# Kernel optimization log

Hardware: AMD Instinct MI355X
Metric: run time of the kernel (lower is better)

## Reference

```python
import jax, jax.numpy as jnp
import numpy as np
from jax.ops import segment_sum

N_NODES = 100000
N_EDGES = 1600000
IN_DIM, HID_DIM, OUT_DIM = 256, 128, 237


def setup_inputs() -> dict:
    key = jax.random.key(0)
    ks = jax.random.split(key, 6)
    x = jax.random.normal(ks[0], (N_NODES, IN_DIM), dtype=jnp.float32)
    edge_index = jax.random.randint(ks[1], (2, N_EDGES), 0, N_NODES, dtype=jnp.int64)
    # Glorot-style init like PyG GCNConv
    W1 = jax.random.normal(ks[2], (IN_DIM, HID_DIM), dtype=jnp.float32) * (1.0 / np.sqrt(IN_DIM))
    b1 = jnp.zeros((HID_DIM,), dtype=jnp.float32)
    W2 = jax.random.normal(ks[3], (HID_DIM, OUT_DIM), dtype=jnp.float32) * (1.0 / np.sqrt(HID_DIM))
    b2 = jnp.zeros((OUT_DIM,), dtype=jnp.float32)
    return {"x": x, "edge_index": edge_index, "W1": W1, "b1": b1, "W2": W2, "b2": b2}


def _gcn_norm(edge_index, num_nodes):
    """Add self-loops and compute symmetric normalization deg^-1/2 * deg^-1/2."""
    loops = jnp.arange(num_nodes, dtype=edge_index.dtype)
    src = jnp.concatenate([edge_index[0], loops])
    dst = jnp.concatenate([edge_index[1], loops])
    deg = segment_sum(jnp.ones_like(dst, dtype=jnp.float32), dst, num_segments=num_nodes)
    dinv = jnp.where(deg > 0, jax.lax.rsqrt(deg), 0.0)
    norm = dinv[src] * dinv[dst]  # [E + N]
    return src, dst, norm


def _gcn_conv(h, src, dst, norm, W, b, num_nodes):
    # PyG GCNConv: linear transform first, then normalized scatter-add aggregation
    hw = h @ W                                   # [N, out]
    msg = hw[src] * norm[:, None]                # gather + scale, [E+N, out]
    out = segment_sum(msg, dst, num_segments=num_nodes)  # scatter-add into dst
    return out + b


def reference(x, edge_index, W1, b1, W2, b2):
    n = x.shape[0]
    src, dst, norm = _gcn_norm(edge_index, n)
    h = _gcn_conv(x, src, dst, norm, W1, b1, n)
    h = jax.nn.relu(h)
    out = _gcn_conv(h, src, dst, norm, W2, b2, n)
    return out
```

## Files before the change

### kernel.cpp

```cpp
#include <hip/hip_runtime.h>

#define N_NODES 100000
#define IN_DIM  256
#define HID_DIM 128
#define OUT_DIM 237

#define BSH   9
#define NBKT  196
#define BNODE 512

typedef __attribute__((ext_vector_type(8))) short bf16x8;
typedef __attribute__((ext_vector_type(4))) float fx4;
typedef __attribute__((ext_vector_type(8))) _Float16 h8;

__global__ __launch_bounds__(256) void k_deg(const int* __restrict__ dst, int* __restrict__ cnt,
                                             int* __restrict__ bcnt, int E) {
    __shared__ int h[NBKT];
    for (int i = threadIdx.x; i < NBKT; i += 256) h[i] = 0;
    __syncthreads();
    const int base = blockIdx.x * 8192;
    for (int it = 0; it < 32; ++it) {
        int e = base + it * 256 + threadIdx.x;
        if (e < E) {
            int d = dst[e];
            atomicAdd(&cnt[d], 1);
            atomicAdd(&h[d >> BSH], 1);
        }
    }
    __syncthreads();
    for (int i = threadIdx.x; i < NBKT; i += 256)
        if (h[i]) atomicAdd(&bcnt[i], h[i]);
}

__global__ void k_dinv(const int* __restrict__ cnt, float* __restrict__ dinv, int n) {
    int i = blockIdx.x * 256 + threadIdx.x;
    if (i < n) dinv[i] = rsqrtf((float)cnt[i] + 1.0f);
}

__global__ __launch_bounds__(256) void k_scan1(const int* __restrict__ cnt,
                                               int* __restrict__ rp,
                                               int* __restrict__ bsum, int n) {
    __shared__ int lds[256];
    const int tid = threadIdx.x;
    const int base = blockIdx.x * 1024 + tid * 4;
    int v[4];
#pragma unroll
    for (int j = 0; j < 4; ++j) v[j] = (base + j < n) ? cnt[base + j] : 0;
    int s = v[0] + v[1] + v[2] + v[3];
    lds[tid] = s;
    __syncthreads();
    for (int off = 1; off < 256; off <<= 1) {
        int t = (tid >= off) ? lds[tid - off] : 0;
        __syncthreads();
        lds[tid] += t;
        __syncthreads();
    }
    int run = lds[tid] - s;
#pragma unroll
    for (int j = 0; j < 4; ++j) {
        if (base + j < n) rp[base + j] = run;
        run += v[j];
    }
    if (tid == 255) bsum[blockIdx.x] = lds[255];
}

__global__ void k_scan2(int* __restrict__ bsum, int nb) {
    __shared__ int lds[128];
    int tid = threadIdx.x;
    int v = (tid < nb) ? bsum[tid] : 0;
    lds[tid] = v;
    __syncthreads();
    for (int off = 1; off < 128; off <<= 1) {
        int t = (tid >= off) ? lds[tid - off] : 0;
        __syncthreads();
        lds[tid] += t;
        __syncthreads();
    }
    if (tid < nb) bsum[tid] = lds[tid] - v;
}

__global__ __launch_bounds__(256) void k_scan3(int* __restrict__ rp,
                                               const int* __restrict__ bsum, int n, int E) {
    const int tid = threadIdx.x;
    const int base = blockIdx.x * 1024 + tid * 4;
    const int add = bsum[blockIdx.x];
#pragma unroll
    for (int j = 0; j < 4; ++j) {
        int i = base + j;
        if (i < n) rp[i] += add;
    }
    if (blockIdx.x == 0 && tid == 0) rp[n] = E;
}

__global__ void k_bscan(const int* __restrict__ bcnt, int* __restrict__ gbase,
                        int* __restrict__ gcur, int E) {
    __shared__ int lds[256];
    int tid = threadIdx.x;
    int v = (tid < NBKT) ? bcnt[tid] : 0;
    lds[tid] = v;
    __syncthreads();
    for (int off = 1; off < 256; off <<= 1) {
        int t = (tid >= off) ? lds[tid - off] : 0;
        __syncthreads();
        lds[tid] += t;
        __syncthreads();
    }
    int excl = lds[tid] - v;
    if (tid < NBKT) { gbase[tid] = excl; gcur[tid] = excl; }
    if (tid == 0) gbase[NBKT] = E;
}

__global__ __launch_bounds__(256) void k_part1(const int* __restrict__ src,
                                               const int* __restrict__ dst,
                                               int* __restrict__ gcur,
                                               int2* __restrict__ pairs, int E) {
    __shared__ int h[NBKT];
    __shared__ int base[NBKT];
    const int tid = threadIdx.x;
    for (int i = tid; i < NBKT; i += 256) h[i] = 0;
    __syncthreads();
    const int cbase = blockIdx.x * 8192;
    for (int it = 0; it < 32; ++it) {
        int e = cbase + it * 256 + tid;
        if (e < E) atomicAdd(&h[dst[e] >> BSH], 1);
    }
    __syncthreads();
    for (int i = tid; i < NBKT; i += 256) {
        int c = h[i];
        base[i] = c ? atomicAdd(&gcur[i], c) : 0;
    }
    __syncthreads();
    for (int i = tid; i < NBKT; i += 256) h[i] = 0;
    __syncthreads();
    for (int it = 0; it < 32; ++it) {
        int e = cbase + it * 256 + tid;
        if (e < E) {
            int d = dst[e];
            int b = d >> BSH;
            int pos = base[b] + atomicAdd(&h[b], 1);
            pairs[pos] = make_int2(src[e], d);
        }
    }
}

__global__ __launch_bounds__(256) void k_part2(const int2* __restrict__ pairs,
                                               const int* __restrict__ gbase,
                                               const int* __restrict__ rp,
                                               int* __restrict__ ss, int n) {
    __shared__ int cur[BNODE];
    const int b = blockIdx.x;
    const int n0 = b << BSH;
    const int tid = threadIdx.x;
    for (int i = tid; i < BNODE; i += 256) {
        int node = n0 + i;
        cur[i] = (node < n) ? rp[node] : 0;
    }
    __syncthreads();
    const int beg = gbase[b], end = gbase[b + 1];
    for (int i = beg + tid; i < end; i += 256) {
        int2 p = pairs[i];
        int pos = atomicAdd(&cur[p.y - n0], 1);
        ss[pos] = p.x;
    }
}

__global__ __launch_bounds__(256) void k_wsplit(const float* __restrict__ W,
                                                unsigned short* __restrict__ Wh,
                                                unsigned short* __restrict__ Wl,
                                                int K, int C, int CD) {
    int t = blockIdx.x * 256 + threadIdx.x;
    if (t >= K * CD) return;
    int k = t / CD, c = t - k * CD;
    float v = (c < C) ? W[k * C + c] : 0.f;
    unsigned u = __float_as_uint(v);
    unsigned short hi = (unsigned short)(u >> 16);
    float lof = v - __uint_as_float(u & 0xffff0000u);
    unsigned short lo = (unsigned short)(__float_as_uint(lof) >> 16);
    int d = ((k >> 3) * CD + c) * 8 + (k & 7);
    Wh[d] = hi;
    Wl[d] = lo;
}

template <typename AT, typename OT, int K, int CD, int SCALE, int BIAS>
__global__ __launch_bounds__(256) void k_gemm_mfma(const AT* __restrict__ A,
                                                   const unsigned short* __restrict__ Bh,
                                                   const unsigned short* __restrict__ Bl,
                                                   const float* __restrict__ dinv,
                                                   const float* __restrict__ bias,
                                                   OT* __restrict__ out,
                                                   int ldo, int ncol) {
    const int tid = threadIdx.x;
    const int lane = tid & 63;
    const int w = tid >> 6;
    const int l15 = lane & 15;
    const int lq = lane >> 4;
    const int rowbase = blockIdx.x * 128 + w * 32;
    const int col0 = blockIdx.y * 128;

    const bf16x8* __restrict__ Bh8 = (const bf16x8*)Bh;
    const bf16x8* __restrict__ Bl8 = (const bf16x8*)Bl;

    fx4 acc[2][8] = {};

    for (int k0 = 0; k0 < K; k0 += 32) {
        bf16x8 ah[2], al[2];
#pragma unroll
        for (int rf = 0; rf < 2; ++rf) {
            int row = rowbase + rf * 16 + l15;
            if (row > N_NODES - 1) row = N_NODES - 1;
            const AT* ap = A + (size_t)row * K + k0 + lq * 8;
            float f[8];
            if constexpr (sizeof(AT) == 4) {
                float4 f0 = *(const float4*)ap;
                float4 f1 = *(const float4*)(ap + 4);
                f[0] = f0.x; f[1] = f0.y; f[2] = f0.z; f[3] = f0.w;
                f[4] = f1.x; f[5] = f1.y; f[6] = f1.z; f[7] = f1.w;
            } else {
                h8 v = *(const h8*)ap;
#pragma unroll
                for (int i = 0; i < 8; ++i) f[i] = (float)v[i];
            }
#pragma unroll
            for (int i = 0; i < 8; ++i) {
                unsigned u = __float_as_uint(f[i]);
                ah[rf][i] = (short)(u >> 16);
                float lof = f[i] - __uint_as_float(u & 0xffff0000u);
                al[rf][i] = (short)(__float_as_uint(lof) >> 16);
            }
        }
        const int kb = (k0 >> 3) + lq;
#pragma unroll
        for (int cf = 0; cf < 8; ++cf) {
            const int bi = kb * CD + col0 + cf * 16 + l15;
            bf16x8 bh = Bh8[bi];
            bf16x8 bl = Bl8[bi];
#pragma unroll
            for (int rf = 0; rf < 2; ++rf) {
                acc[rf][cf] = __builtin_amdgcn_mfma_f32_16x16x32_bf16(ah[rf], bh, acc[rf][cf], 0, 0, 0);
                acc[rf][cf] = __builtin_amdgcn_mfma_f32_16x16x32_bf16(ah[rf], bl, acc[rf][cf], 0, 0, 0);
                acc[rf][cf] = __builtin_amdgcn_mfma_f32_16x16x32_bf16(al[rf], bh, acc[rf][cf], 0, 0, 0);
            }
        }
    }

    float bb[8];
#pragma unroll
    for (int cf = 0; cf < 8; ++cf) {
        int c = col0 + cf * 16 + l15;
        bb[cf] = (BIAS && c < ncol) ? bias[c] : 0.f;
    }

#pragma unroll
    for (int rf = 0; rf < 2; ++rf) {
#pragma unroll
        for (int r = 0; r < 4; ++r) {
            const int row = rowbase + rf * 16 + lq * 4 + r;
            if (row < N_NODES) {
                const float s = SCALE ? dinv[row] : 1.f;
#pragma unroll
                for (int cf = 0; cf < 8; ++cf) {
                    const int c = col0 + cf * 16 + l15;
                    if (c < ncol) {
                        float v = acc[rf][cf][r];
                        if (SCALE) v *= s;
                        if (BIAS) v += bb[cf];
                        out[(size_t)row * ldo + c] = (OT)v;
                    }
                }
            }
        }
    }
}

template <int RELU, typename OT>
__global__ __launch_bounds__(256) void k_agg_csr(const _Float16* __restrict__ tab,
                                                 const int* __restrict__ rp,
                                                 const int* __restrict__ ss,
                                                 const float* __restrict__ dinv,
                                                 const float* __restrict__ bias,
                                                 OT* __restrict__ outp, int n) {
    int t = blockIdx.x * 256 + threadIdx.x;
    int node = t >> 4;
    int q = (t & 15) * 8;
    if (node >= n) return;
    int beg = rp[node], end = rp[node + 1];
    float a[8] = {};
    int i = beg;
    for (; i + 2 <= end; i += 2) {
        int s0 = ss[i], s1 = ss[i + 1];
        h8 v0 = *(const h8*)(tab + (size_t)s0 * HID_DIM + q);
        h8 v1 = *(const h8*)(tab + (size_t)s1 * HID_DIM + q);
#pragma unroll
        for (int j = 0; j < 8; ++j) a[j] += (float)v0[j] + (float)v1[j];
    }
    if (i < end) {
        int s0 = ss[i];
        h8 v0 = *(const h8*)(tab + (size_t)s0 * HID_DIM + q);
#pragma unroll
        for (int j = 0; j < 8; ++j) a[j] += (float)v0[j];
    }
    h8 own = *(const h8*)(tab + (size_t)node * HID_DIM + q);
    float s = dinv[node];
    if constexpr (RELU) {
        float4 b0 = *(const float4*)(bias + q);
        float4 b1 = *(const float4*)(bias + q + 4);
        float bb[8] = {b0.x, b0.y, b0.z, b0.w, b1.x, b1.y, b1.z, b1.w};
        h8 r;
#pragma unroll
        for (int j = 0; j < 8; ++j)
            r[j] = (_Float16)(fmaxf(fmaf(s, a[j] + (float)own[j], bb[j]), 0.f) * s);
        *(h8*)((_Float16*)outp + (size_t)node * HID_DIM + q) = r;
    } else if constexpr (sizeof(OT) == 2) {
        h8 r;
#pragma unroll
        for (int j = 0; j < 8; ++j) r[j] = (_Float16)(s * (a[j] + (float)own[j]));
        *(h8*)((_Float16*)outp + (size_t)node * HID_DIM + q) = r;
    } else {
        float* op = (float*)outp + (size_t)node * HID_DIM + q;
        float4 r0, r1;
        r0.x = s * (a[0] + (float)own[0]);
        r0.y = s * (a[1] + (float)own[1]);
        r0.z = s * (a[2] + (float)own[2]);
        r0.w = s * (a[3] + (float)own[3]);
        r1.x = s * (a[4] + (float)own[4]);
        r1.y = s * (a[5] + (float)own[5]);
        r1.z = s * (a[6] + (float)own[6]);
        r1.w = s * (a[7] + (float)own[7]);
        *(float4*)op = r0;
        *(float4*)(op + 4) = r1;
    }
}

__global__ __launch_bounds__(256) void k_gemm2(const float* __restrict__ A2,
                                               const float* __restrict__ W2,
                                               const float* __restrict__ b2,
                                               float* __restrict__ out) {
    __shared__ float As[16 * 132];
    __shared__ float Bs[16 * 128];
    const int tid = threadIdx.x;
    const int tx = tid & 15, ty = tid >> 4;
    const int row0 = blockIdx.x * 128;
    const int col0 = blockIdx.y * 128;

    const int ar = tid >> 2;
    const int ak = (tid & 3) * 4;
    const int bk = tid >> 5;
    const int bc = (tid & 31) * 4;

    float acc[8][8] = {};

    for (int k0 = 0; k0 < HID_DIM; k0 += 16) {
        float4 a0 = make_float4(0.f, 0.f, 0.f, 0.f), a1 = a0;
        const int r0 = row0 + ar, r1 = row0 + ar + 64;
        if (r0 < N_NODES) a0 = *(const float4*)(A2 + (size_t)r0 * HID_DIM + k0 + ak);
        if (r1 < N_NODES) a1 = *(const float4*)(A2 + (size_t)r1 * HID_DIM + k0 + ak);
        float bv0[4], bv1[4];
#pragma unroll
        for (int j = 0; j < 4; ++j) {
            int c = col0 + bc + j;
            bv0[j] = (c < OUT_DIM) ? W2[(size_t)(k0 + bk) * OUT_DIM + c] : 0.f;
            bv1[j] = (c < OUT_DIM) ? W2[(size_t)(k0 + bk + 8) * OUT_DIM + c] : 0.f;
        }
        __syncthreads();
        As[(ak + 0) * 132 + ar] = a0.x;
        As[(ak + 1) * 132 + ar] = a0.y;
        As[(ak + 2) * 132 + ar] = a0.z;
        As[(ak + 3) * 132 + ar] = a0.w;
        As[(ak + 0) * 132 + ar + 64] = a1.x;
        As[(ak + 1) * 132 + ar + 64] = a1.y;
        As[(ak + 2) * 132 + ar + 64] = a1.z;
        As[(ak + 3) * 132 + ar + 64] = a1.w;
#pragma unroll
        for (int j = 0; j < 4; ++j) {
            Bs[bk * 128 + bc + j] = bv0[j];
            Bs[(bk + 8) * 128 + bc + j] = bv1[j];
        }
        __syncthreads();
#pragma unroll
        for (int kk = 0; kk < 16; ++kk) {
            float4 A0 = *(const float4*)(As + kk * 132 + ty * 4);
            float4 A1 = *(const float4*)(As + kk * 132 + 64 + ty * 4);
            float4 B0 = *(const float4*)(Bs + kk * 128 + tx * 4);
            float4 B1 = *(const float4*)(Bs + kk * 128 + 64 + tx * 4);
            float a_[8] = {A0.x, A0.y, A0.z, A0.w, A1.x, A1.y, A1.z, A1.w};
            float b_[8] = {B0.x, B0.y, B0.z, B0.w, B1.x, B1.y, B1.z, B1.w};
#pragma unroll
            for (int i = 0; i < 8; ++i)
#pragma unroll
                for (int j = 0; j < 8; ++j)
                    acc[i][j] = fmaf(a_[i], b_[j], acc[i][j]);
        }
    }
#pragma unroll
    for (int i = 0; i < 8; ++i) {
        const int r = row0 + ty * 4 + (i & 3) + (i >> 2) * 64;
        if (r < N_NODES) {
#pragma unroll
            for (int j = 0; j < 8; ++j) {
                int c = col0 + tx * 4 + (j & 3) + (j >> 2) * 64;
                if (c < OUT_DIM) out[(size_t)r * OUT_DIM + c] = acc[i][j] + b2[c];
            }
        }
    }
}

extern "C" void kernel_launch(void* const* d_in, const int* in_sizes, int n_in,
                              void* d_out, int out_size, void* d_ws, size_t ws_size,
                              hipStream_t stream) {
    const float* x  = (const float*)d_in[0];
    const int*   ei = (const int*)d_in[1];
    const float* W1 = (const float*)d_in[2];
    const float* b1 = (const float*)d_in[3];
    const float* W2 = (const float*)d_in[4];
    const float* b2 = (const float*)d_in[5];
    float* out = (float*)d_out;

    const int E = in_sizes[1] / 2;
    const int* src = ei;
    const int* dst = ei + E;

    _Float16* hs = (_Float16*)d_ws;
    _Float16* A2h = hs;
    float* A2f = (float*)d_ws;

    char* ob = (char*)d_out;
    size_t o = (size_t)N_NODES * HID_DIM * 2;
    _Float16* h2 = (_Float16*)ob;
    float* dinv = (float*)(ob + o); o += 400128;
    int* cnt  = (int*)(ob + o); o += 400128;
    int* bcnt = (int*)(ob + o); o += 1024;
    int* rp   = (int*)(ob + o); o += 400640;
    int* bsum = (int*)(ob + o); o += 1024;
    int* gbase = (int*)(ob + o); o += 1024;
    int* gcur  = (int*)(ob + o); o += 1024;
    int* ss   = (int*)(ob + o); o += (size_t)E * 4;
    int2* pairs = (int2*)(ob + o); o += (size_t)E * 8;
    unsigned short* W1h = (unsigned short*)(ob + o); o += 65536;
    unsigned short* W1l = (unsigned short*)(ob + o); o += 65536;

    const size_t W2OFF = 32u << 20;
    const bool w2frag = ws_size >= W2OFF + 131072;
    unsigned short* W2h = (unsigned short*)((char*)d_ws + W2OFF);
    unsigned short* W2l = W2h + 32768;

    const int NB  = (N_NODES + 1023) / 1024;
    const int NB1 = (E + 8191) / 8192;

    k_wsplit<<<128, 256, 0, stream>>>(W1, W1h, W1l, IN_DIM, HID_DIM, HID_DIM);
    if (w2frag)
        k_wsplit<<<128, 256, 0, stream>>>(W2, W2h, W2l, HID_DIM, OUT_DIM, 256);

    hipMemsetAsync(cnt, 0, 400128 + 1024, stream);
    k_deg<<<NB1, 256, 0, stream>>>(dst, cnt, bcnt, E);
    k_dinv<<<(N_NODES + 255) / 256, 256, 0, stream>>>(cnt, dinv, N_NODES);
    k_scan1<<<NB, 256, 0, stream>>>(cnt, rp, bsum, N_NODES);
    k_scan2<<<1, 128, 0, stream>>>(bsum, NB);
    k_scan3<<<NB, 256, 0, stream>>>(rp, bsum, N_NODES, E);
    k_bscan<<<1, 256, 0, stream>>>(bcnt, gbase, gcur, E);
    k_part1<<<NB1, 256, 0, stream>>>(src, dst, gcur, pairs, E);
    k_part2<<<NBKT, 256, 0, stream>>>(pairs, gbase, rp, ss, N_NODES);

    dim3 g1((N_NODES + 127) / 128, 1);
    k_gemm_mfma<float, _Float16, IN_DIM, HID_DIM, 1, 0><<<g1, 256, 0, stream>>>(
        x, W1h, W1l, dinv, nullptr, hs, HID_DIM, HID_DIM);

    const int aggBlocks = (N_NODES * 16 + 255) / 256;
    k_agg_csr<1, _Float16><<<aggBlocks, 256, 0, stream>>>(hs, rp, ss, dinv, b1, h2, N_NODES);

    if (w2frag) {
        k_agg_csr<0, _Float16><<<aggBlocks, 256, 0, stream>>>(h2, rp, ss, dinv, b1, A2h, N_NODES);
        dim3 g2((N_NODES + 127) / 128, 2);
        k_gemm_mfma<_Float16, float, HID_DIM, 256, 0, 1><<<g2, 256, 0, stream>>>(
            A2h, W2h, W2l, nullptr, b2, out, OUT_DIM, OUT_DIM);
    } else {
        k_agg_csr<0, float><<<aggBlocks, 256, 0, stream>>>(h2, rp, ss, dinv, b1, A2f, N_NODES);
        dim3 g2((N_NODES + 127) / 128, (OUT_DIM + 127) / 128);
        k_gemm2<<<g2, 256, 0, stream>>>(A2f, W2, b2, out);
    }
}
```

Baseline: 541.2 us.

## Derive per-node degrees and CSR offsets inside bucket partition kernel

Drops the global per-node degree atomics, the dinv kernel and the three-pass global scan. Each bucket block now counts its nodes' in-degrees in LDS from the partitioned pairs, scans them locally, and writes row pointers and dinv before scattering sources. This removes 1.6M global atomics and several launches. In exchange, the 196 bucket blocks read the pairs array twice and carry more serial work.

```diff
diff --git a/kernel.cpp b/kernel.cpp
--- a/kernel.cpp
+++ b/kernel.cpp
@@ -13,83 +13,19 @@
 typedef __attribute__((ext_vector_type(4))) float fx4;
 typedef __attribute__((ext_vector_type(8))) _Float16 h8;
 
-__global__ __launch_bounds__(256) void k_deg(const int* __restrict__ dst, int* __restrict__ cnt,
-                                             int* __restrict__ bcnt, int E) {
+__global__ __launch_bounds__(256) void k_bhist(const int* __restrict__ dst,
+                                               int* __restrict__ bcnt, int E) {
     __shared__ int h[NBKT];
     for (int i = threadIdx.x; i < NBKT; i += 256) h[i] = 0;
     __syncthreads();
     const int base = blockIdx.x * 8192;
     for (int it = 0; it < 32; ++it) {
         int e = base + it * 256 + threadIdx.x;
-        if (e < E) {
-            int d = dst[e];
-            atomicAdd(&cnt[d], 1);
-            atomicAdd(&h[d >> BSH], 1);
-        }
+        if (e < E) atomicAdd(&h[dst[e] >> BSH], 1);
     }
     __syncthreads();
     for (int i = threadIdx.x; i < NBKT; i += 256)
         if (h[i]) atomicAdd(&bcnt[i], h[i]);
-}
-
-__global__ void k_dinv(const int* __restrict__ cnt, float* __restrict__ dinv, int n) {
-    int i = blockIdx.x * 256 + threadIdx.x;
-    if (i < n) dinv[i] = rsqrtf((float)cnt[i] + 1.0f);
-}
-
-__global__ __launch_bounds__(256) void k_scan1(const int* __restrict__ cnt,
-                                               int* __restrict__ rp,
-                                               int* __restrict__ bsum, int n) {
-    __shared__ int lds[256];
-    const int tid = threadIdx.x;
-    const int base = blockIdx.x * 1024 + tid * 4;
-    int v[4];
-#pragma unroll
-    for (int j = 0; j < 4; ++j) v[j] = (base + j < n) ? cnt[base + j] : 0;
-    int s = v[0] + v[1] + v[2] + v[3];
-    lds[tid] = s;
-    __syncthreads();
-    for (int off = 1; off < 256; off <<= 1) {
-        int t = (tid >= off) ? lds[tid - off] : 0;
-        __syncthreads();
-        lds[tid] += t;
-        __syncthreads();
-    }
-    int run = lds[tid] - s;
-#pragma unroll
-    for (int j = 0; j < 4; ++j) {
-        if (base + j < n) rp[base + j] = run;
-        run += v[j];
-    }
-    if (tid == 255) bsum[blockIdx.x] = lds[255];
-}
-
-__global__ void k_scan2(int* __restrict__ bsum, int nb) {
-    __shared__ int lds[128];
-    int tid = threadIdx.x;
-    int v = (tid < nb) ? bsum[tid] : 0;
-    lds[tid] = v;
-    __syncthreads();
-    for (int off = 1; off < 128; off <<= 1) {
-        int t = (tid >= off) ? lds[tid - off] : 0;
-        __syncthreads();
-        lds[tid] += t;
-        __syncthreads();
-    }
-    if (tid < nb) bsum[tid] = lds[tid] - v;
-}
-
-__global__ __launch_bounds__(256) void k_scan3(int* __restrict__ rp,
-                                               const int* __restrict__ bsum, int n, int E) {
-    const int tid = threadIdx.x;
-    const int base = blockIdx.x * 1024 + tid * 4;
-    const int add = bsum[blockIdx.x];
-#pragma unroll
-    for (int j = 0; j < 4; ++j) {
-        int i = base + j;
-        if (i < n) rp[i] += add;
-    }
-    if (blockIdx.x == 0 && tid == 0) rp[n] = E;
 }
 
 __global__ void k_bscan(const int* __restrict__ bcnt, int* __restrict__ gbase,
@@ -143,25 +79,53 @@
     }
 }
 
-__global__ __launch_bounds__(256) void k_part2(const int2* __restrict__ pairs,
-                                               const int* __restrict__ gbase,
-                                               const int* __restrict__ rp,
-                                               int* __restrict__ ss, int n) {
-    __shared__ int cur[BNODE];
+__global__ __launch_bounds__(256) void k_bucket_csr(const int2* __restrict__ pairs,
+                                                    const int* __restrict__ gbase,
+                                                    int* __restrict__ rp,
+                                                    float* __restrict__ dinv,
+                                                    int* __restrict__ ss, int n, int E) {
+    __shared__ int cnt[BNODE];
+    __shared__ int excl[BNODE];
+    __shared__ int sbuf[256];
     const int b = blockIdx.x;
     const int n0 = b << BSH;
     const int tid = threadIdx.x;
+    for (int i = tid; i < BNODE; i += 256) cnt[i] = 0;
+    __syncthreads();
+    const int beg = gbase[b], end = gbase[b + 1];
+    for (int i = beg + tid; i < end; i += 256)
+        atomicAdd(&cnt[pairs[i].y - n0], 1);
+    __syncthreads();
+    int c0 = cnt[2 * tid], c1 = cnt[2 * tid + 1];
+    int s = c0 + c1;
+    sbuf[tid] = s;
+    __syncthreads();
+    for (int off = 1; off < 256; off <<= 1) {
+        int t = (tid >= off) ? sbuf[tid - off] : 0;
+        __syncthreads();
+        sbuf[tid] += t;
+        __syncthreads();
+    }
+    int e0 = sbuf[tid] - s;
+    excl[2 * tid] = e0;
+    excl[2 * tid + 1] = e0 + c0;
+    __syncthreads();
     for (int i = tid; i < BNODE; i += 256) {
         int node = n0 + i;
-        cur[i] = (node < n) ? rp[node] : 0;
-    }
-    __syncthreads();
-    const int beg = gbase[b], end = gbase[b + 1];
+        if (node < n) {
+            rp[node] = beg + excl[i];
+            dinv[node] = rsqrtf((float)cnt[i] + 1.0f);
+        }
+    }
+    __syncthreads();
+    for (int i = tid; i < BNODE; i += 256) cnt[i] = beg + excl[i];
+    __syncthreads();
     for (int i = beg + tid; i < end; i += 256) {
         int2 p = pairs[i];
-        int pos = atomicAdd(&cur[p.y - n0], 1);
+        int pos = atomicAdd(&cnt[p.y - n0], 1);
         ss[pos] = p.x;
     }
+    if (b == 0 && tid == 0) rp[n] = E;
 }
 
 __global__ __launch_bounds__(256) void k_wsplit(const float* __restrict__ W,
@@ -427,10 +391,8 @@
     size_t o = (size_t)N_NODES * HID_DIM * 2;
     _Float16* h2 = (_Float16*)ob;
     float* dinv = (float*)(ob + o); o += 400128;
-    int* cnt  = (int*)(ob + o); o += 400128;
     int* bcnt = (int*)(ob + o); o += 1024;
     int* rp   = (int*)(ob + o); o += 400640;
-    int* bsum = (int*)(ob + o); o += 1024;
     int* gbase = (int*)(ob + o); o += 1024;
     int* gcur  = (int*)(ob + o); o += 1024;
     int* ss   = (int*)(ob + o); o += (size_t)E * 4;
@@ -443,22 +405,17 @@
     unsigned short* W2h = (unsigned short*)((char*)d_ws + W2OFF);
     unsigned short* W2l = W2h + 32768;
 
-    const int NB  = (N_NODES + 1023) / 1024;
     const int NB1 = (E + 8191) / 8192;
 
     k_wsplit<<<128, 256, 0, stream>>>(W1, W1h, W1l, IN_DIM, HID_DIM, HID_DIM);
     if (w2frag)
         k_wsplit<<<128, 256, 0, stream>>>(W2, W2h, W2l, HID_DIM, OUT_DIM, 256);
 
-    hipMemsetAsync(cnt, 0, 400128 + 1024, stream);
-    k_deg<<<NB1, 256, 0, stream>>>(dst, cnt, bcnt, E);
-    k_dinv<<<(N_NODES + 255) / 256, 256, 0, stream>>>(cnt, dinv, N_NODES);
-    k_scan1<<<NB, 256, 0, stream>>>(cnt, rp, bsum, N_NODES);
-    k_scan2<<<1, 128, 0, stream>>>(bsum, NB);
-    k_scan3<<<NB, 256, 0, stream>>>(rp, bsum, N_NODES, E);
+    hipMemsetAsync(bcnt, 0, 1024, stream);
+    k_bhist<<<NB1, 256, 0, stream>>>(dst, bcnt, E);
     k_bscan<<<1, 256, 0, stream>>>(bcnt, gbase, gcur, E);
     k_part1<<<NB1, 256, 0, stream>>>(src, dst, gcur, pairs, E);
-    k_part2<<<NBKT, 256, 0, stream>>>(pairs, gbase, rp, ss, N_NODES);
+    k_bucket_csr<<<NBKT, 256, 0, stream>>>(pairs, gbase, rp, dinv, ss, N_NODES, E);
 
     dim3 g1((N_NODES + 127) / 128, 1);
     k_gemm_mfma<float, _Float16, IN_DIM, HID_DIM, 1, 0><<<g1, 256, 0, stream>>>(
```

New measurement: 488.3 us. -9.8%, faster.
